# Kernel tuning notes

Hardware: AMD Instinct MI355X
Metric: run time of the kernel (lower is better)

Reference implementation:

```python
import jax, jax.numpy as jnp
import numpy as np


def _igd(x, pf):
    # pf: [M, d] reference front, x: [N, d] candidate set
    # squared Euclidean distances via ||a||^2 + ||b||^2 - 2 a.b (cdist expansion)
    pf_sq = jnp.sum(pf * pf, axis=1, keepdims=True)          # [M, 1]
    x_sq = jnp.sum(x * x, axis=1, keepdims=True).T            # [1, N]
    cross = pf @ x.T                                          # [M, N]
    d2 = jnp.maximum(pf_sq + x_sq - 2.0 * cross, 0.0)
    dist = jnp.sqrt(d2)                                       # [M, N]
    # IGD: mean over reference points of min distance to candidate set
    return jnp.mean(jnp.min(dist, axis=1))


def setup_inputs() -> dict:
    key = jax.random.key(0)
    k1, k2 = jax.random.split(key)
    N, M, D = 16384, 16384, 64
    x = jax.random.normal(k1, (N, D), dtype=jnp.float32)
    pf = jax.random.normal(k2, (M, D), dtype=jnp.float32)
    return {"x": x, "pf": pf}


def reference(x, pf):
    return _igd(x, pf)
```

## Files before the change

kernel.cpp:

```cpp
#include <hip/hip_runtime.h>


typedef float f32x16 __attribute__((ext_vector_type(16)));
typedef int i32x8 __attribute__((ext_vector_type(8)));
typedef unsigned long long u64;

#define DIM 64
#define NSPLIT 12
#define UNITB 2048
#define CHUNKU 8
#define CHUNKB (CHUNKU * UNITB)
#define MTILE 256

union BFrag { u64 q[4]; i32x8 v; };

__device__ __forceinline__ void g2lds16(const void* g, void* l) {
    __builtin_amdgcn_global_load_lds(
        (const __attribute__((address_space(1))) unsigned int*)g,
        (__attribute__((address_space(3))) unsigned int*)l, 16, 0, 0);
}
__device__ __forceinline__ void g2lds4(const void* g, void* l) {
    __builtin_amdgcn_global_load_lds(
        (const __attribute__((address_space(1))) unsigned int*)g,
        (__attribute__((address_space(3))) unsigned int*)l, 4, 0, 0);
}

__device__ inline unsigned char enc_e4m3(float f) {
    unsigned int u = __float_as_uint(f);
    unsigned int s = (u >> 24) & 0x80u;
    unsigned int a = u & 0x7FFFFFFFu;
    if ((a >> 23) >= 121u) {
        unsigned int lsb = (a >> 20) & 1u;
        unsigned int r = a + 0x7FFFFu + lsb;
        int e = (int)(r >> 23) - 120;
        unsigned int m = (r >> 20) & 7u;
        if (e > 15 || (e == 15 && m == 7u)) return (unsigned char)(s | 0x7Eu);
        return (unsigned char)(s | ((unsigned)e << 3) | m);
    }
    int m = (int)rintf(__uint_as_float(a) * 512.0f);
    return (unsigned char)(s | (unsigned)m);
}

__device__ inline float dec_e4m3(unsigned char b) {
    int e = (b >> 3) & 15, m = b & 7;
    float v = e ? __uint_as_float((unsigned)((e + 120) << 23) | ((unsigned)m << 20))
                : (float)m * 0.001953125f;
    return (b & 0x80) ? -v : v;
}

__global__ void pack_kernel(const float* __restrict__ x, const float* __restrict__ pf,
                            unsigned char* __restrict__ Bp, unsigned char* __restrict__ Ab,
                            float* __restrict__ xsq, float* __restrict__ pfsq,
                            float* __restrict__ out, int N, int M) {
    int gid = blockIdx.x * blockDim.x + threadIdx.x;
    if (gid == 0) out[0] = 0.f;
    if (gid < N * 4) {
        int col = gid >> 2, t = gid & 3;
        const float* s = x + (size_t)col * DIM + t * 16;
        float partial = 0.f;
        u64 w[2] = {0, 0};
#pragma unroll
        for (int h = 0; h < 2; ++h) {
            float4 v0 = *(const float4*)(s + h * 8);
            float4 v1 = *(const float4*)(s + h * 8 + 4);
            float f[8] = {v0.x, v0.y, v0.z, v0.w, v1.x, v1.y, v1.z, v1.w};
#pragma unroll
            for (int j = 0; j < 8; ++j) {
                unsigned char b = enc_e4m3(f[j]);
                w[h] |= (u64)b << (8 * j);
                float d = dec_e4m3(b);
                partial += d * d;
            }
        }
        int u = col >> 5, c31 = col & 31;
        unsigned char* ub = Bp + (size_t)u * UNITB;
        int h = t >> 1;
#pragma unroll
        for (int ss = 0; ss < 2; ++ss) {
            int q = (t & 1) * 2 + ss;
            *(u64*)(ub + (size_t)q * 512 + (size_t)(h * 32 + c31) * 8) = w[ss];
        }
        partial += __shfl_xor(partial, 1);
        partial += __shfl_xor(partial, 2);
        if (t == 0) xsq[col] = partial;
    } else {
        int g = gid - N * 4;
        int row = g >> 2, q = g & 3;
        if (row >= M) return;
        const float* s = pf + (size_t)row * DIM + q * 16;
        float partial = 0.f;
        u64 w[2] = {0, 0};
#pragma unroll
        for (int h = 0; h < 2; ++h) {
            float4 v0 = *(const float4*)(s + h * 8);
            float4 v1 = *(const float4*)(s + h * 8 + 4);
            float f[8] = {v0.x, v0.y, v0.z, v0.w, v1.x, v1.y, v1.z, v1.w};
#pragma unroll
            for (int j = 0; j < 8; ++j) {
                unsigned char b = enc_e4m3(f[j] * -2.f);
                w[h] |= (u64)b << (8 * j);
                float d = dec_e4m3(b);
                partial += d * d;
            }
        }
        *(u64*)(Ab + (size_t)row * DIM + q * 16)     = w[0];
        *(u64*)(Ab + (size_t)row * DIM + q * 16 + 8) = w[1];
        partial += __shfl_xor(partial, 1);
        partial += __shfl_xor(partial, 2);
        if (q == 0) pfsq[row] = partial * 0.25f;
    }
}

__global__ __launch_bounds__(256, 3)
void igd_main(const unsigned char* __restrict__ A, const unsigned char* __restrict__ Bp,
              const float* __restrict__ xsq, float* __restrict__ partial, int N) {
    __shared__ unsigned char ldsB[2][CHUNKB];
    __shared__ float ldsX[2][CHUNKU * 32];
    const int tid = threadIdx.x;
    const int mTile  = blockIdx.x;
    const int nsplit = blockIdx.y;
    const int lane = tid & 63;
    const int wave = tid >> 6;
    const int half = lane >> 5;
    const int l31  = lane & 31;
    const int rowBase = mTile * MTILE + wave * 64;

    const int utotal = N / 32;
    const int ubase  = utotal / NSPLIT;
    const int urem   = utotal % NSPLIT;
    const int ustart = nsplit * ubase + (nsplit < urem ? nsplit : urem);
    const int ucount = ubase + (nsplit < urem ? 1 : 0);
    const int nch = (ucount + CHUNKU - 1) / CHUNKU;

    BFrag a[2];
#pragma unroll
    for (int g = 0; g < 2; ++g) {
        const unsigned char* ap = A + (size_t)(rowBase + 32 * g + l31) * DIM + half * 32;
#pragma unroll
        for (int qq = 0; qq < 4; ++qq)
            a[g].q[qq] = *(const u64*)(ap + qq * 8);
    }

    const unsigned char* gB = Bp + (size_t)ustart * UNITB;
    const float* gX = xsq + ustart * 32;

#define STAGE(c, buf)                                                          \
    {                                                                          \
        int bytes = (ucount - (c) * CHUNKU) < CHUNKU ? (ucount - (c) * CHUNKU) * UNITB : CHUNKB; \
        const unsigned char* src = gB + (size_t)(c) * CHUNKB;                  \
        _Pragma("unroll")                                                      \
        for (int i = 0; i < 4; ++i) {                                          \
            int off = i * 4096 + tid * 16;                                     \
            if (off < bytes)                                                   \
                g2lds16(src + off, &ldsB[buf][off]);                           \
        }                                                                      \
        int xcnt = bytes >> 6;                                                 \
        if (tid < xcnt)                                                        \
            g2lds4(gX + (c) * (CHUNKU * 32) + tid, &ldsX[buf][tid]);           \
    }

    f32x16 zero, m0, m1;
#pragma unroll
    for (int r = 0; r < 16; ++r) { zero[r] = 0.f; m0[r] = 1e30f; m1[r] = 1e30f; }

#define LOADF(rr, lb, u)                                                       \
    {                                                                          \
        const unsigned char* p = (lb) + (u) * UNITB;                           \
        rr.q[0] = *(const u64*)(p);                                            \
        rr.q[1] = *(const u64*)(p + 512);                                      \
        rr.q[2] = *(const u64*)(p + 1024);                                     \
        rr.q[3] = *(const u64*)(p + 1536);                                     \
    }

#define MFMA2(accA, accB, bfrag)                                               \
    {                                                                          \
        accA = __builtin_amdgcn_mfma_scale_f32_32x32x64_f8f6f4(                \
            a[0].v, bfrag.v, zero, 0, 0, 0, 0x7F7F7F7F, 0, 0x7F7F7F7F);        \
        accB = __builtin_amdgcn_mfma_scale_f32_32x32x64_f8f6f4(                \
            a[1].v, bfrag.v, zero, 0, 0, 0, 0x7F7F7F7F, 0, 0x7F7F7F7F);        \
    }

#define MINS(accA, accB, xq)                                                   \
    {                                                                          \
        _Pragma("unroll")                                                      \
        for (int r = 0; r < 16; ++r) {                                         \
            m0[r] = fminf(m0[r], accA[r] + (xq));                              \
            m1[r] = fminf(m1[r], accB[r] + (xq));                              \
        }                                                                      \
    }

    STAGE(0, 0);
    __syncthreads();

    for (int c = 0; c < nch; ++c) {
        const int buf = c & 1;
        if (c + 1 < nch) STAGE(c + 1, buf ^ 1);
        const int cnt = (ucount - c * CHUNKU) < CHUNKU ? (ucount - c * CHUNKU) : CHUNKU;
        const unsigned char* lb = &ldsB[buf][0] + lane * 8;
        const float* lx = &ldsX[buf][0] + l31;
        if (cnt == CHUNKU) {
            BFrag b0, b1;
            LOADF(b0, lb, 0);
#pragma unroll
            for (int u = 0; u < CHUNKU; u += 2) {
                LOADF(b1, lb, u + 1);
                f32x16 acA0, acA1;
                MFMA2(acA0, acA1, b0);
                MINS(acA0, acA1, lx[u * 32]);
                if (u + 2 < CHUNKU) LOADF(b0, lb, u + 2);
                f32x16 acB0, acB1;
                MFMA2(acB0, acB1, b1);
                MINS(acB0, acB1, lx[(u + 1) * 32]);
            }
        } else {
            BFrag bt;
            for (int u = 0; u < cnt; ++u) {
                LOADF(bt, lb, u);
                f32x16 t0, t1;
                MFMA2(t0, t1, bt);
                MINS(t0, t1, lx[u * 32]);
            }
        }
        __syncthreads();
    }
#undef STAGE
#undef LOADF
#undef MFMA2
#undef MINS

#pragma unroll
    for (int mask = 1; mask <= 16; mask <<= 1) {
#pragma unroll
        for (int r = 0; r < 16; ++r) {
            m0[r] = fminf(m0[r], __shfl_xor(m0[r], mask));
            m1[r] = fminf(m1[r], __shfl_xor(m1[r], mask));
        }
    }
    if (l31 == 0) {
#pragma unroll
        for (int r = 0; r < 16; ++r) {
            int row0 = rowBase + (r & 3) + 8 * (r >> 2) + 4 * half;
            partial[(size_t)row0 * NSPLIT + nsplit] = m0[r];
            partial[(size_t)(row0 + 32) * NSPLIT + nsplit] = m1[r];
        }
    }
}

__global__ void reduce_kernel(const float* __restrict__ partial, const float* __restrict__ pfsq,
                              float* __restrict__ out, int M, float invM) {
    int row = blockIdx.x * blockDim.x + threadIdx.x;
    float v = 0.f;
    if (row < M) {
        const float* p = partial + (size_t)row * NSPLIT;
        float mn = 3.4e38f;
#pragma unroll
        for (int s = 0; s < NSPLIT; ++s) mn = fminf(mn, p[s]);
        float d2 = mn + pfsq[row];
        v = sqrtf(fmaxf(d2, 0.f)) * invM;
    }
#pragma unroll
    for (int m = 1; m < 64; m <<= 1) v += __shfl_xor(v, m);
    __shared__ float wsum[4];
    int lane = threadIdx.x & 63, w = threadIdx.x >> 6;
    if (lane == 0) wsum[w] = v;
    __syncthreads();
    if (threadIdx.x == 0) atomicAdd(out, wsum[0] + wsum[1] + wsum[2] + wsum[3]);
}

extern "C" void kernel_launch(void* const* d_in, const int* in_sizes, int n_in,
                              void* d_out, int out_size, void* d_ws, size_t ws_size,
                              hipStream_t stream) {
    const float* x  = (const float*)d_in[0];
    const float* pf = (const float*)d_in[1];
    const int N = in_sizes[0] / DIM;
    const int M = in_sizes[1] / DIM;

    char* ws = (char*)d_ws;
    unsigned char* Bp = (unsigned char*)ws;
    unsigned char* Ab = (unsigned char*)(ws + (size_t)N * DIM);
    float* xsq  = (float*)(ws + (size_t)(N + M) * DIM);
    float* pfsq = xsq + N;
    float* part = pfsq + M;

    int packThreads = (N + M) * 4;
    pack_kernel<<<dim3((packThreads + 255) / 256), 256, 0, stream>>>(
        x, pf, Bp, Ab, xsq, pfsq, (float*)d_out, N, M);
    igd_main<<<dim3(M / MTILE, NSPLIT), 256, 0, stream>>>(Ab, Bp, xsq, part, N);
    reduce_kernel<<<dim3((M + 255) / 256), 256, 0, stream>>>(part, pfsq, (float*)d_out, M, 1.f / (float)M);
}
```

Measured before the change: 90.25 us.

## Use 512-thread blocks with one 32-row MFMA tile per wave

Each wave now handles 32 reference rows instead of 64, and blocks grow to 8 waves so the 256-row tile stays the same. Each wave issues one MFMA per B fragment instead of two, and the per-thread register footprint for accumulators and min buffers is halved, allowing higher occupancy. The trade-off is that each B fragment read from LDS is reused by only one MFMA per wave, so LDS read traffic per FLOP doubles. Fewer independent MFMAs per wave also gives less instruction-level parallelism to hide latency.

```diff
diff --git a/kernel.cpp b/kernel.cpp
--- a/kernel.cpp
+++ b/kernel.cpp
@@ -111,7 +111,7 @@
     }
 }
 
-__global__ __launch_bounds__(256, 3)
+__global__ __launch_bounds__(512, 6)
 void igd_main(const unsigned char* __restrict__ A, const unsigned char* __restrict__ Bp,
               const float* __restrict__ xsq, float* __restrict__ partial, int N) {
     __shared__ unsigned char ldsB[2][CHUNKB];
@@ -123,7 +123,7 @@
     const int wave = tid >> 6;
     const int half = lane >> 5;
     const int l31  = lane & 31;
-    const int rowBase = mTile * MTILE + wave * 64;
+    const int rowBase = mTile * MTILE + wave * 32;
 
     const int utotal = N / 32;
     const int ubase  = utotal / NSPLIT;
@@ -132,13 +132,12 @@
     const int ucount = ubase + (nsplit < urem ? 1 : 0);
     const int nch = (ucount + CHUNKU - 1) / CHUNKU;
 
-    BFrag a[2];
-#pragma unroll
-    for (int g = 0; g < 2; ++g) {
-        const unsigned char* ap = A + (size_t)(rowBase + 32 * g + l31) * DIM + half * 32;
+    BFrag a;
+    {
+        const unsigned char* ap = A + (size_t)(rowBase + l31) * DIM + half * 32;
 #pragma unroll
         for (int qq = 0; qq < 4; ++qq)
-            a[g].q[qq] = *(const u64*)(ap + qq * 8);
+            a.q[qq] = *(const u64*)(ap + qq * 8);
     }
 
     const unsigned char* gB = Bp + (size_t)ustart * UNITB;
@@ -149,8 +148,8 @@
         int bytes = (ucount - (c) * CHUNKU) < CHUNKU ? (ucount - (c) * CHUNKU) * UNITB : CHUNKB; \
         const unsigned char* src = gB + (size_t)(c) * CHUNKB;                  \
         _Pragma("unroll")                                                      \
-        for (int i = 0; i < 4; ++i) {                                          \
-            int off = i * 4096 + tid * 16;                                     \
+        for (int i = 0; i < 2; ++i) {                                          \
+            int off = i * 8192 + tid * 16;                                     \
             if (off < bytes)                                                   \
                 g2lds16(src + off, &ldsB[buf][off]);                           \
         }                                                                      \
@@ -159,9 +158,9 @@
             g2lds4(gX + (c) * (CHUNKU * 32) + tid, &ldsX[buf][tid]);           \
     }
 
-    f32x16 zero, m0, m1;
-#pragma unroll
-    for (int r = 0; r < 16; ++r) { zero[r] = 0.f; m0[r] = 1e30f; m1[r] = 1e30f; }
+    f32x16 zero, m0;
+#pragma unroll
+    for (int r = 0; r < 16; ++r) { zero[r] = 0.f; m0[r] = 1e30f; }
 
 #define LOADF(rr, lb, u)                                                       \
     {                                                                          \
@@ -172,21 +171,13 @@
         rr.q[3] = *(const u64*)(p + 1536);                                     \
     }
 
-#define MFMA2(accA, accB, bfrag)                                               \
+#define STEP(bfrag, xq)                                                        \
     {                                                                          \
-        accA = __builtin_amdgcn_mfma_scale_f32_32x32x64_f8f6f4(                \
-            a[0].v, bfrag.v, zero, 0, 0, 0, 0x7F7F7F7F, 0, 0x7F7F7F7F);        \
-        accB = __builtin_amdgcn_mfma_scale_f32_32x32x64_f8f6f4(                \
-            a[1].v, bfrag.v, zero, 0, 0, 0, 0x7F7F7F7F, 0, 0x7F7F7F7F);        \
-    }
-
-#define MINS(accA, accB, xq)                                                   \
-    {                                                                          \
+        f32x16 acc = __builtin_amdgcn_mfma_scale_f32_32x32x64_f8f6f4(          \
+            a.v, bfrag.v, zero, 0, 0, 0, 0x7F7F7F7F, 0, 0x7F7F7F7F);           \
         _Pragma("unroll")                                                      \
-        for (int r = 0; r < 16; ++r) {                                         \
-            m0[r] = fminf(m0[r], accA[r] + (xq));                              \
-            m1[r] = fminf(m1[r], accB[r] + (xq));                              \
-        }                                                                      \
+        for (int r = 0; r < 16; ++r)                                           \
+            m0[r] = fminf(m0[r], acc[r] + (xq));                               \
     }
 
     STAGE(0, 0);
@@ -204,44 +195,34 @@
 #pragma unroll
             for (int u = 0; u < CHUNKU; u += 2) {
                 LOADF(b1, lb, u + 1);
-                f32x16 acA0, acA1;
-                MFMA2(acA0, acA1, b0);
-                MINS(acA0, acA1, lx[u * 32]);
+                STEP(b0, lx[u * 32]);
                 if (u + 2 < CHUNKU) LOADF(b0, lb, u + 2);
-                f32x16 acB0, acB1;
-                MFMA2(acB0, acB1, b1);
-                MINS(acB0, acB1, lx[(u + 1) * 32]);
+                STEP(b1, lx[(u + 1) * 32]);
             }
         } else {
             BFrag bt;
             for (int u = 0; u < cnt; ++u) {
                 LOADF(bt, lb, u);
-                f32x16 t0, t1;
-                MFMA2(t0, t1, bt);
-                MINS(t0, t1, lx[u * 32]);
+                STEP(bt, lx[u * 32]);
             }
         }
         __syncthreads();
     }
 #undef STAGE
 #undef LOADF
-#undef MFMA2
-#undef MINS
+#undef STEP
 
 #pragma unroll
     for (int mask = 1; mask <= 16; mask <<= 1) {
 #pragma unroll
-        for (int r = 0; r < 16; ++r) {
+        for (int r = 0; r < 16; ++r)
             m0[r] = fminf(m0[r], __shfl_xor(m0[r], mask));
-            m1[r] = fminf(m1[r], __shfl_xor(m1[r], mask));
-        }
     }
     if (l31 == 0) {
 #pragma unroll
         for (int r = 0; r < 16; ++r) {
             int row0 = rowBase + (r & 3) + 8 * (r >> 2) + 4 * half;
             partial[(size_t)row0 * NSPLIT + nsplit] = m0[r];
-            partial[(size_t)(row0 + 32) * NSPLIT + nsplit] = m1[r];
         }
     }
 }
@@ -285,6 +266,6 @@
     int packThreads = (N + M) * 4;
     pack_kernel<<<dim3((packThreads + 255) / 256), 256, 0, stream>>>(
         x, pf, Bp, Ab, xsq, pfsq, (float*)d_out, N, M);
-    igd_main<<<dim3(M / MTILE, NSPLIT), 256, 0, stream>>>(Ab, Bp, xsq, part, N);
+    igd_main<<<dim3(M / MTILE, NSPLIT), 512, 0, stream>>>(Ab, Bp, xsq, part, N);
     reduce_kernel<<<dim3((M + 255) / 256), 256, 0, stream>>>(part, pfsq, (float*)d_out, M, 1.f / (float)M);
 }
```

Result: slower. 106.9 us (+18.5%).
